# Optimization experiments

Hardware: AMD Instinct MI355X
Metric: run time of the kernel (lower is better)

## Reference

```python
import jax, jax.numpy as jnp
import numpy as np

B, T1, T2 = 2, 1024, 512
D_MODEL, N_HEAD, D_HEAD = 1024, 16, 64
SCALE = 1.0 / D_HEAD ** 0.5
EPS = 1e-5


def _skew(qe):
    # qe: [B, H, T, 2T-1] -> [B, H, T, T] via Transformer-XL pad/reshape trick
    b, h, t, x = qe.shape
    qe = jnp.pad(qe, ((0, 0), (0, 0), (0, 0), (0, 1))).reshape(b, h, 2 * t * t)
    qe = jnp.pad(qe, ((0, 0), (0, 0), (0, t - 1))).reshape(b, h, t + 1, 2 * t - 1)
    return qe[:, :, :t, -t:]


def setup_inputs() -> dict:
    key = jax.random.key(0)
    ks = jax.random.split(key, 12)
    s = 0.02
    return {
        "Q": jax.random.normal(ks[0], (B, T1, D_MODEL), jnp.float32),
        "K": jax.random.normal(ks[1], (B, T1, D_MODEL), jnp.float32),
        "V": jax.random.normal(ks[2], (B, T1, D_MODEL), jnp.float32),
        "lookup_table": jax.random.normal(ks[3], (2 * T1 - 1, D_HEAD), jnp.float32) * s,
        "valid_frames": jnp.sort(jax.random.randint(ks[4], (T2,), 0, T1)),
        "mask": jax.random.bernoulli(ks[5], 0.1, (B, N_HEAD, T1, T2)),
        "Wq": jax.random.normal(ks[6], (D_MODEL, N_HEAD * D_HEAD), jnp.float32) * s,
        "Wk": jax.random.normal(ks[7], (D_MODEL, N_HEAD * D_HEAD), jnp.float32) * s,
        "Wv": jax.random.normal(ks[8], (D_MODEL, N_HEAD * D_HEAD), jnp.float32) * s,
        "Wo": jax.random.normal(ks[9], (N_HEAD * D_HEAD, D_MODEL), jnp.float32) * s,
        "bo": jnp.zeros((D_MODEL,), jnp.float32),
        "ln_g": jnp.ones((D_MODEL,), jnp.float32),
        "ln_b": jnp.zeros((D_MODEL,), jnp.float32),
    }


def reference(Q, K, V, lookup_table, valid_frames, mask, Wq, Wk, Wv, Wo, bo, ln_g, ln_b):
    # gather valid KV frames (raw inputs, before projection)
    K = K[:, valid_frames]  # [B, T2, D]
    V = V[:, valid_frames]
    # pre-layernorm on Q only
    mu = jnp.mean(Q, axis=-1, keepdims=True)
    var = jnp.var(Q, axis=-1, keepdims=True)
    Qn = (Q - mu) * jax.lax.rsqrt(var + EPS) * ln_g + ln_b
    # projections -> [B, H, T, d_head]
    q = (Qn @ Wq).reshape(B, T1, N_HEAD, D_HEAD).transpose(0, 2, 1, 3)
    k = (K @ Wk).reshape(B, T2, N_HEAD, D_HEAD).transpose(0, 2, 1, 3)
    v = (V @ Wv).reshape(B, T2, N_HEAD, D_HEAD).transpose(0, 2, 1, 3)
    # content score + skewed relative-position score
    score = jnp.einsum("bhqd,bhkd->bhqk", q, k)  # [B,H,T1,T2]
    rel = jnp.einsum("bhqd,xd->bhqx", q, lookup_table)  # [B,H,T1,2T1-1]
    rel = _skew(rel)[:, :, :, valid_frames]  # [B,H,T1,T2]
    score = (score + rel) * SCALE
    score = jnp.where(mask, -jnp.finfo(score.dtype).max, score)
    attn = jax.nn.softmax(score, axis=-1)
    ctx = jnp.einsum("bhqk,bhkd->bhqd", attn, v)
    ctx = ctx.transpose(0, 2, 1, 3).reshape(B, T1, N_HEAD * D_HEAD)
    out = ctx @ Wo + bo  # dropout is identity at inference
    return out + ctx  # pre_layernorm=True branch
```

## Files before the change

kernel.cpp:

```cpp
#include <hip/hip_runtime.h>
#include <stdint.h>
#include <stddef.h>

typedef __attribute__((ext_vector_type(8))) short s16x8;
typedef __attribute__((ext_vector_type(4))) short s16x4;
typedef __attribute__((ext_vector_type(4))) float f32x4;

#define MFMA(a,b,c) __builtin_amdgcn_mfma_f32_16x16x32_bf16((a),(b),(c),0,0,0)

static __device__ __forceinline__ unsigned short f2b(float f){
  unsigned int b = __float_as_uint(f);
  b = (b + 0x7FFFu + ((b>>16)&1u)) >> 16;
  return (unsigned short)b;
}
static __device__ __forceinline__ float b2f(unsigned short u){
  return __uint_as_float(((unsigned int)u)<<16);
}


__global__ __launch_bounds__(256) void k_mask(const unsigned char* __restrict__ m,
    unsigned int* __restrict__ MB){
  const int t = threadIdx.x;
  const size_t g0 = (size_t)blockIdx.x*16;
  __shared__ int cnt1, cnt23;
  if(t==0){ cnt1=0; cnt23=0; }
  __syncthreads();
  const uint4* bp = (const uint4*)(m + g0*512);
  int l1=0,l23=0;
  #pragma unroll
  for(int i=0;i<2;i++){
    uint4 v = bp[t + i*256];
    unsigned int ws[4] = {v.x,v.y,v.z,v.w};
    #pragma unroll
    for(int j=0;j<4;j++){
      if((ws[j]>>8)&0xFFu) l1++;
      if(ws[j]>>16)        l23++;
    }
  }
  #pragma unroll
  for(int o=1;o<64;o<<=1){ l1 += __shfl_xor(l1,o); l23 += __shfl_xor(l23,o); }
  if((t&63)==0){ atomicAdd(&cnt1,l1); atomicAdd(&cnt23,l23); }
  __syncthreads();
  const int flag = cnt1 ? 1 : (cnt23 ? 2 : 0);

  const int rl = t>>4, f = t&15;
  const size_t base = (g0 + rl)*512 + f;
  unsigned int word = 0;
  if(flag==0){
    const int* p = (const int*)m;
    #pragma unroll
    for(int i=0;i<32;i++) word |= (p[base+i*16]!=0 ? 1u:0u) << i;
  } else if(flag==1){
    #pragma unroll
    for(int i=0;i<32;i++) word |= (m[base+i*16]!=0 ? 1u:0u) << i;
  } else {
    const float* p = (const float*)m;
    #pragma unroll
    for(int i=0;i<32;i++) word |= (p[base+i*16]!=0.f ? 1u:0u) << i;
  }
  MB[((size_t)blockIdx.x*4 + (t>>6))*64 + f*4 + (rl&3)] = word;
}

__global__ __launch_bounds__(256) void k_prep(
    const float* __restrict__ Q, const float* __restrict__ g, const float* __restrict__ be,
    unsigned short* __restrict__ Qn,
    const float* __restrict__ K, const float* __restrict__ V, const int* __restrict__ vf,
    unsigned short* __restrict__ Kg, unsigned short* __restrict__ Vg,
    const float* __restrict__ L, unsigned short* __restrict__ Lb,
    const float* __restrict__ W0, const float* __restrict__ W1,
    const float* __restrict__ W2, const float* __restrict__ W3,
    unsigned short* __restrict__ D0, unsigned short* __restrict__ D1,
    unsigned short* __restrict__ D2, unsigned short* __restrict__ D3){
  __shared__ float tile[64][65];
  __shared__ float red[8];
  const int bid = blockIdx.x, t = threadIdx.x;
  if(bid < 2048){
    const float4* xp = (const float4*)(Q + (size_t)bid*1024);
    float4 v = xp[t];
    float s  = v.x+v.y+v.z+v.w;
    float s2 = v.x*v.x+v.y*v.y+v.z*v.z+v.w*v.w;
    #pragma unroll
    for(int o=1;o<64;o<<=1){ s += __shfl_xor(s,o); s2 += __shfl_xor(s2,o); }
    int w = t>>6, l = t&63;
    if(l==0){ red[w]=s; red[4+w]=s2; }
    __syncthreads();
    s  = red[0]+red[1]+red[2]+red[3];
    s2 = red[4]+red[5]+red[6]+red[7];
    float mu = s*(1.f/1024.f);
    float var = s2*(1.f/1024.f) - mu*mu;
    float rs = rsqrtf(var + 1e-5f);
    float4 gv = ((const float4*)g)[t];
    float4 bv = ((const float4*)be)[t];
    ushort4 o4;
    o4.x = f2b((v.x-mu)*rs*gv.x + bv.x);
    o4.y = f2b((v.y-mu)*rs*gv.y + bv.y);
    o4.z = f2b((v.z-mu)*rs*gv.z + bv.z);
    o4.w = f2b((v.w-mu)*rs*gv.w + bv.w);
    ((ushort4*)(Qn + (size_t)bid*1024))[t] = o4;
  } else if(bid < 4096){
    int row = bid - 2048;
    int isV = row>>10, r = row&1023;
    int b = r>>9, jj = r&511;
    const float* src = (isV? V : K) + ((size_t)(b*1024 + vf[jj]))*1024;
    unsigned short* dst = (isV? Vg : Kg) + (size_t)r*1024;
    float4 v = ((const float4*)src)[t];
    ushort4 o; o.x=f2b(v.x); o.y=f2b(v.y); o.z=f2b(v.z); o.w=f2b(v.w);
    ((ushort4*)dst)[t] = o;
  } else if(bid < 4608){
    int i = (bid-4096)*256 + t;
    if(i < 2047*64) Lb[i] = f2b(L[i]);
  } else {
    int idx = bid - 4608;
    int z = idx>>8, rem = idx&255;
    int k0 = (rem&15)*64, n0 = (rem>>4)*64;
    const float* S = z==0?W0: z==1?W1: z==2?W2:W3;
    unsigned short* D = z==0?D0: z==1?D1: z==2?D2:D3;
    int tr = t>>6, tc = t&63;
    #pragma unroll
    for(int it=0;it<16;it++){ int r = it*4+tr; tile[r][tc] = S[(size_t)(k0+r)*1024 + n0+tc]; }
    __syncthreads();
    #pragma unroll
    for(int it=0;it<16;it++){ int r = it*4+tr; D[(size_t)(n0+r)*1024 + k0+tc] = f2b(tile[tc][r]); }
  }
}

__global__ __launch_bounds__(256) void k_proj(
    const short* __restrict__ QN, const short* __restrict__ WQT,
    const short* __restrict__ KG, const short* __restrict__ WKT,
    const short* __restrict__ WVT, const short* __restrict__ VG,
    unsigned short* __restrict__ QB, unsigned short* __restrict__ KB,
    unsigned short* __restrict__ VT){
  __shared__ __align__(16) short Ab[128*32];
  __shared__ __align__(16) short Bb[128*32];
  int bid = blockIdx.x;
  int mode, bx;
  if(bid<128){ mode=0; bx=bid>>3; }
  else if(bid<192){ mode=1; bx=(bid-128)>>3; }
  else { mode=2; bx=(bid-192)>>3; }
  int by = bid&7;
  const short* A  = mode==0? QN : mode==1? KG : WVT;
  const short* Bt = mode==0? WQT: mode==1? WKT: VG;

  const int t = threadIdx.x;
  const int w = t>>6, l = t&63;
  const int wr = w>>1, wc = w&1;
  const int fl15 = l&15, fl4 = l>>4;
  const size_t m0 = (size_t)bx*128, n0 = (size_t)by*128;
  const int srow = t>>2, scb = t&3;
  const int sg = scb ^ ((srow>>1)&3);
  const short* Ap = A + (m0+srow)*1024 + 8*sg;
  const short* Bp = Bt + (n0+srow)*1024 + 8*sg;

  f32x4 acc[4][4];
  const f32x4 zero = {0.f,0.f,0.f,0.f};
  #pragma unroll
  for(int m=0;m<4;m++)
    #pragma unroll
    for(int n=0;n<4;n++) acc[m][n] = zero;

  for(int k0=0;k0<1024;k0+=32){
    s16x8 a0 = *(const s16x8*)(Ap + k0);
    s16x8 a1 = *(const s16x8*)(Ap + 64*1024 + k0);
    s16x8 b0 = *(const s16x8*)(Bp + k0);
    s16x8 b1 = *(const s16x8*)(Bp + 64*1024 + k0);
    __syncthreads();
    *(s16x8*)(Ab + srow*32 + scb*8)      = a0;
    *(s16x8*)(Ab + (64+srow)*32 + scb*8) = a1;
    *(s16x8*)(Bb + srow*32 + scb*8)      = b0;
    *(s16x8*)(Bb + (64+srow)*32 + scb*8) = b1;
    __syncthreads();
    s16x8 af[4], bff[4];
    #pragma unroll
    for(int m=0;m<4;m++){
      int row = wr*64 + m*16 + fl15;
      int gg = fl4 ^ ((row>>1)&3);
      af[m] = *(const s16x8*)(Ab + row*32 + gg*8);
    }
    #pragma unroll
    for(int n=0;n<4;n++){
      int row = wc*64 + n*16 + fl15;
      int gg = fl4 ^ ((row>>1)&3);
      bff[n] = *(const s16x8*)(Bb + row*32 + gg*8);
    }
    #pragma unroll
    for(int m=0;m<4;m++)
      #pragma unroll
      for(int n=0;n<4;n++)
        acc[m][n] = MFMA(af[m], bff[n], acc[m][n]);
  }

  #pragma unroll
  for(int m=0;m<4;m++){
    #pragma unroll
    for(int n=0;n<4;n++){
      int mgb = (int)m0 + wr*64 + m*16 + 4*fl4;
      int ng  = (int)n0 + wc*64 + n*16 + fl15;
      #pragma unroll
      for(int p=0;p<4;p++){
        int mg = mgb + p;
        float v = acc[m][n][p];
        if(mode==0){ int b=mg>>10, i=mg&1023, h=ng>>6, d=ng&63;
          QB[((size_t)((b*16+h)*1024+i))*64 + d] = f2b(v); }
        else if(mode==1){ int b=mg>>9, jj=mg&511, h=ng>>6, d=ng&63;
          KB[((size_t)((b*16+h)*512+jj))*64 + d] = f2b(v); }
        else { int h=mg>>6, d=mg&63, b=ng>>9, jj=ng&511;
          VT[((size_t)((b*16+h)*64+d))*512 + jj] = f2b(v); }
      }
    }
  }
}

__global__ __launch_bounds__(256) void k_gemmO(
    const short* __restrict__ A, const short* __restrict__ Bt,
    float* __restrict__ out, const float* __restrict__ bo,
    const float* __restrict__ ctxf){
  __shared__ __align__(16) short Ab[128*32];
  __shared__ __align__(16) short Bb[128*32];
  const int t = threadIdx.x;
  const int w = t>>6, l = t&63;
  const int wr = w>>1, wc = w&1;
  const int fl15 = l&15, fl4 = l>>4;
  const size_t m0 = (size_t)blockIdx.x*128, n0 = (size_t)blockIdx.y*128;
  const int srow = t>>2, scb = t&3;
  const int sg = scb ^ ((srow>>1)&3);
  const short* Ap = A + (m0+srow)*1024 + 8*sg;
  const short* Bp = Bt + (n0+srow)*1024 + 8*sg;

  f32x4 acc[4][4];
  const f32x4 zero = {0.f,0.f,0.f,0.f};
  #pragma unroll
  for(int m=0;m<4;m++)
    #pragma unroll
    for(int n=0;n<4;n++) acc[m][n] = zero;

  for(int k0=0;k0<1024;k0+=32){
    s16x8 a0 = *(const s16x8*)(Ap + k0);
    s16x8 a1 = *(const s16x8*)(Ap + 64*1024 + k0);
    s16x8 b0 = *(const s16x8*)(Bp + k0);
    s16x8 b1 = *(const s16x8*)(Bp + 64*1024 + k0);
    __syncthreads();
    *(s16x8*)(Ab + srow*32 + scb*8)      = a0;
    *(s16x8*)(Ab + (64+srow)*32 + scb*8) = a1;
    *(s16x8*)(Bb + srow*32 + scb*8)      = b0;
    *(s16x8*)(Bb + (64+srow)*32 + scb*8) = b1;
    __syncthreads();
    s16x8 af[4], bff[4];
    #pragma unroll
    for(int m=0;m<4;m++){
      int row = wr*64 + m*16 + fl15;
      int gg = fl4 ^ ((row>>1)&3);
      af[m] = *(const s16x8*)(Ab + row*32 + gg*8);
    }
    #pragma unroll
    for(int n=0;n<4;n++){
      int row = wc*64 + n*16 + fl15;
      int gg = fl4 ^ ((row>>1)&3);
      bff[n] = *(const s16x8*)(Bb + row*32 + gg*8);
    }
    #pragma unroll
    for(int m=0;m<4;m++)
      #pragma unroll
      for(int n=0;n<4;n++)
        acc[m][n] = MFMA(af[m], bff[n], acc[m][n]);
  }

  #pragma unroll
  for(int m=0;m<4;m++){
    #pragma unroll
    for(int n=0;n<4;n++){
      int mgb = (int)m0 + wr*64 + m*16 + 4*fl4;
      int ng  = (int)n0 + wc*64 + n*16 + fl15;
      #pragma unroll
      for(int p=0;p<4;p++){
        int mg = mgb + p;
        size_t idx = (size_t)mg*1024 + ng;
        out[idx] = acc[m][n][p] + bo[ng] + ctxf[idx];
      }
    }
  }
}

#define RGS 20
#define GROWS 287
__global__ __launch_bounds__(256,2) void k_attn(const short* __restrict__ qb,
    const short* __restrict__ kb, const short* __restrict__ vt,
    const short* __restrict__ lbf, const int* __restrict__ vf,
    const unsigned int* __restrict__ MB,
    unsigned short* __restrict__ ctxb, float* __restrict__ ctxf){
  __shared__ __align__(16) short Gs[4][GROWS*RGS];
  __shared__ __align__(16) short PB[4][1024];
  __shared__ int vfs[512];
  const int t=threadIdx.x, w=t>>6, l=t&63, fl15=l&15, fl4=l>>4;
  const int bh = blockIdx.y;
  const int qg = blockIdx.x;
  const int qw = qg*16;
  for(int i=t;i<512;i+=256) vfs[i]=vf[i];
  __syncthreads();
  const int vf0 = vfs[0];
  const int x0  = 1008 + vf0 - qw;
  const int xcw = x0 + w*256;

  const short* qp = qb + ((size_t)(bh*1024 + qw + fl15))*64 + 8*fl4;
  s16x8 qa0 = *(const s16x8*)qp;
  s16x8 qa1 = *(const s16x8*)(qp+32);

  short* Gw = &Gs[w][0];
  const f32x4 zero = {0.f,0.f,0.f,0.f};
  #pragma unroll 4
  for(int tt=0;tt<17;tt++){
    int xr = xcw + tt*16 + fl15; if(xr>2046) xr = 2046;
    const short* lp = lbf + (size_t)xr*64 + 8*fl4;
    s16x8 b0 = *(const s16x8*)lp;
    s16x8 b1 = *(const s16x8*)(lp+32);
    f32x4 a = zero;
    a = MFMA(qa0,b0,a); a = MFMA(qa1,b1,a);
    int cb = tt*16 + fl15 + 4*fl4;
    #pragma unroll
    for(int p=0;p<4;p++) Gw[(cb+p)*RGS + 4*fl4 + p] = (short)f2b(a[p]);
  }

  const int rowgrp = bh*256 + qg*4 + fl4;
  uint4 mv = ((const uint4*)MB)[rowgrp*16 + fl15];
  unsigned int mbits[4] = {mv.x, mv.y, mv.z, mv.w};

  __syncthreads();

  const short* kp_row = kb + ((size_t)(bh*512 + fl15))*64 + 8*fl4;
  const short* vpb[4];
  #pragma unroll
  for(int dt=0;dt<4;dt++)
    vpb[dt] = vt + ((size_t)(bh*64 + dt*16 + fl15))*512 + w*128 + 8*fl4;

  f32x4 facc[4];
  #pragma unroll
  for(int dt=0;dt<4;dt++) facc[dt] = zero;
  float m_run[4] = {-1e30f,-1e30f,-1e30f,-1e30f};
  float ps[4]    = {0.f,0.f,0.f,0.f};
  short* Pw = &PB[w][0];

  for(int c=0;c<2;c++){
    s16x8 vfr[8];
    #pragma unroll
    for(int dt=0;dt<4;dt++){
      vfr[2*dt]   = *(const s16x8*)(vpb[dt] + c*64);
      vfr[2*dt+1] = *(const s16x8*)(vpb[dt] + c*64 + 32);
    }
    f32x4 S[4];
    #pragma unroll
    for(int tl=0;tl<4;tl++){
      int ttg = 8*w + 4*c + tl;
      const short* ka = kp_row + (size_t)ttg*1024;
      s16x8 k0v = *(const s16x8*)ka;
      s16x8 k1v = *(const s16x8*)(ka+32);
      f32x4 a = zero;
      a = MFMA(qa0,k0v,a); a = MFMA(qa1,k1v,a);
      int jj = ttg*16 + fl15;
      int o  = vfs[jj] - vf0;
      s16x4 rl = *(const s16x4*)(&Gs[o>>8][((o&255)+15)*RGS + 4*fl4]);
      #pragma unroll
      for(int p=0;p<4;p++){
        float sv = (a[p] + b2f((unsigned short)rl[p])) * 0.125f;
        bool mskb = (mbits[p]>>ttg)&1u;
        a[p] = mskb ? -1e30f : sv;
      }
      S[tl] = a;
    }
    float cm[4];
    #pragma unroll
    for(int p=0;p<4;p++){
      cm[p] = fmaxf(fmaxf(S[0][p],S[1][p]), fmaxf(S[2][p],S[3][p]));
      #pragma unroll
      for(int o=1;o<16;o<<=1) cm[p] = fmaxf(cm[p], __shfl_xor(cm[p],o));
      float mn = fmaxf(m_run[p], cm[p]);
      float fac = __expf(m_run[p]-mn);
      m_run[p] = mn;
      ps[p] *= fac;
      #pragma unroll
      for(int dt=0;dt<4;dt++) facc[dt][p] *= fac;
    }
    #pragma unroll
    for(int tl=0;tl<4;tl++){
      #pragma unroll
      for(int p=0;p<4;p++){
        float e = __expf(S[tl][p]-m_run[p]);
        ps[p] += e;
        int row = 4*fl4+p;
        Pw[row*64 + ((tl*16 + fl15) ^ (fl4<<4))] = (short)f2b(e);
      }
    }
    #pragma unroll
    for(int s=0;s<2;s++){
      s16x8 pa = *(const s16x8*)(Pw + fl15*64 + ((s*32 + fl4*8) ^ ((fl15>>2)<<4)));
      #pragma unroll
      for(int dt=0;dt<4;dt++)
        facc[dt] = MFMA(pa, vfr[2*dt+s], facc[dt]);
    }
  }

  #pragma unroll
  for(int p=0;p<4;p++){
    #pragma unroll
    for(int o=1;o<16;o<<=1) ps[p] += __shfl_xor(ps[p],o);
  }

  __syncthreads();
  float* MT = (float*)&Gs[0][0];
  float* ST = MT + 64;
  float* MG = ST + 64;
  if(fl15==0){
    #pragma unroll
    for(int p=0;p<4;p++){ MT[w*16 + 4*fl4+p] = m_run[p]; ST[w*16 + 4*fl4+p] = ps[p]; }
  }
  __syncthreads();
  float scale[4];
  #pragma unroll
  for(int p=0;p<4;p++){
    int row = 4*fl4+p;
    float ms  = fmaxf(fmaxf(MT[row],MT[16+row]), fmaxf(MT[32+row],MT[48+row]));
    float den = __expf(MT[row]-ms)*ST[row] + __expf(MT[16+row]-ms)*ST[16+row]
              + __expf(MT[32+row]-ms)*ST[32+row] + __expf(MT[48+row]-ms)*ST[48+row];
    scale[p] = __expf(m_run[p]-ms) / den;
  }
  #pragma unroll
  for(int dt=0;dt<4;dt++)
    #pragma unroll
    for(int p=0;p<4;p++)
      MG[(w*16 + 4*fl4+p)*65 + dt*16 + fl15] = facc[dt][p]*scale[p];
  __syncthreads();
  const int b = bh>>4, h = bh&15;
  #pragma unroll
  for(int p=0;p<4;p++){
    int row = 4*fl4+p;
    float v = MG[(row)*65    + w*16+fl15] + MG[(16+row)*65 + w*16+fl15]
            + MG[(32+row)*65 + w*16+fl15] + MG[(48+row)*65 + w*16+fl15];
    size_t idx = ((size_t)(b*1024 + qw + row))*1024 + h*64 + w*16 + fl15;
    ctxb[idx] = f2b(v);
    ctxf[idx] = v;
  }
}

extern "C" void kernel_launch(void* const* d_in, const int* in_sizes, int n_in,
                              void* d_out, int out_size, void* d_ws, size_t ws_size,
                              hipStream_t stream){
  (void)in_sizes; (void)n_in; (void)out_size; (void)ws_size;
  const float* Q  = (const float*)d_in[0];
  const float* K  = (const float*)d_in[1];
  const float* V  = (const float*)d_in[2];
  const float* Lt = (const float*)d_in[3];
  const int*   vf = (const int*)d_in[4];
  const void*  mk = d_in[5];
  const float* Wq = (const float*)d_in[6];
  const float* Wk = (const float*)d_in[7];
  const float* Wv = (const float*)d_in[8];
  const float* Wo = (const float*)d_in[9];
  const float* bo = (const float*)d_in[10];
  const float* lg = (const float*)d_in[11];
  const float* lb = (const float*)d_in[12];

  char* base = (char*)d_ws;
  size_t off = 0;
  auto alloc = [&](size_t bytes)->char*{
    char* p = base + off; off += (bytes + 255) & ~(size_t)255; return p; };
  unsigned int*   MBp = (unsigned int*)alloc(32768ull*16*4);
  unsigned short* QN  = (unsigned short*)alloc(2048ull*1024*2);
  unsigned short* KG  = (unsigned short*)alloc(1024ull*1024*2);
  unsigned short* VG  = (unsigned short*)alloc(1024ull*1024*2);
  unsigned short* WQT = (unsigned short*)alloc(1024ull*1024*2);
  unsigned short* WKT = (unsigned short*)alloc(1024ull*1024*2);
  unsigned short* WVT = (unsigned short*)alloc(1024ull*1024*2);
  unsigned short* WOT = (unsigned short*)alloc(1024ull*1024*2);
  unsigned short* LB  = (unsigned short*)alloc(2047ull*64*2);
  unsigned short* QB  = (unsigned short*)alloc(32ull*1024*64*2);
  unsigned short* KB  = (unsigned short*)alloc(32ull*512*64*2);
  unsigned short* VT  = (unsigned short*)alloc(32ull*64*512*2);
  unsigned short* CB  = (unsigned short*)alloc(2048ull*1024*2);
  float*          CF  = (float*)alloc(2048ull*1024*4);

  k_mask<<<2048,256,0,stream>>>((const unsigned char*)mk, MBp);
  k_prep<<<5632,256,0,stream>>>(Q, lg, lb, QN, K, V, vf, KG, VG, Lt, LB,
                                Wq, Wk, Wv, Wo, WQT, WKT, WVT, WOT);
  k_proj<<<256,256,0,stream>>>((const short*)QN,(const short*)WQT,
                               (const short*)KG,(const short*)WKT,
                               (const short*)WVT,(const short*)VG,
                               QB, KB, VT);
  k_attn<<<dim3(64,32),256,0,stream>>>((const short*)QB,(const short*)KB,(const short*)VT,
                                       (const short*)LB, vf, MBp, CB, CF);
  k_gemmO<<<dim3(16,8),256,0,stream>>>((const short*)CB,(const short*)WOT,
                                       (float*)d_out, bo, CF);
}
```

Before: 146.0 us.

## Split attention keys across eight waves per block and drop online softmax loop

The attention kernel now launches 512 threads per block, so each of eight waves handles 64 keys in a single pass rather than four waves looping over two 64-key chunks. K fragments are prefetched into registers before the relative-position table build, and that build is split across wave halves. The P buffer now reuses the Gs shared region after an extra barrier, and the cross-wave softmax merge is widened to eight partials. This adds parallelism and latency hiding per block but raises register pressure and adds barriers under a 512,4 launch bound.

Measured after the change: 144.9 us. Within noise of the previous version (-0.8%).

```diff
diff --git a/kernel.cpp b/kernel.cpp
--- a/kernel.cpp
+++ b/kernel.cpp
@@ -282,32 +282,45 @@
 
 #define RGS 20
 #define GROWS 287
-__global__ __launch_bounds__(256,2) void k_attn(const short* __restrict__ qb,
+__global__ __launch_bounds__(512,4) void k_attn(const short* __restrict__ qb,
     const short* __restrict__ kb, const short* __restrict__ vt,
     const short* __restrict__ lbf, const int* __restrict__ vf,
     const unsigned int* __restrict__ MB,
     unsigned short* __restrict__ ctxb, float* __restrict__ ctxf){
   __shared__ __align__(16) short Gs[4][GROWS*RGS];
-  __shared__ __align__(16) short PB[4][1024];
   __shared__ int vfs[512];
   const int t=threadIdx.x, w=t>>6, l=t&63, fl15=l&15, fl4=l>>4;
   const int bh = blockIdx.y;
   const int qg = blockIdx.x;
   const int qw = qg*16;
-  for(int i=t;i<512;i+=256) vfs[i]=vf[i];
-  __syncthreads();
-  const int vf0 = vfs[0];
-  const int x0  = 1008 + vf0 - qw;
-  const int xcw = x0 + w*256;
 
   const short* qp = qb + ((size_t)(bh*1024 + qw + fl15))*64 + 8*fl4;
   s16x8 qa0 = *(const s16x8*)qp;
   s16x8 qa1 = *(const s16x8*)(qp+32);
-
-  short* Gw = &Gs[w][0];
+  const int rowgrp = bh*256 + qg*4 + fl4;
+  uint4 mv = ((const uint4*)MB)[rowgrp*16 + fl15];
+
+  const short* kp_row = kb + ((size_t)(bh*512 + fl15))*64 + 8*fl4;
+  s16x8 kf[8];
+  #pragma unroll
+  for(int i=0;i<4;i++){
+    const short* ka = kp_row + (size_t)(4*w+i)*1024;
+    kf[2*i]   = *(const s16x8*)ka;
+    kf[2*i+1] = *(const s16x8*)(ka+32);
+  }
+
+  vfs[t] = vf[t & 511];
+  __syncthreads();
+  const int vf0 = vfs[0];
+  const int x0  = 1008 + vf0 - qw;
+  const int cw  = w&3;
+  const int xcw = x0 + cw*256;
+
+  short* Gw = &Gs[cw][0];
   const f32x4 zero = {0.f,0.f,0.f,0.f};
-  #pragma unroll 4
-  for(int tt=0;tt<17;tt++){
+  const int tbeg = (w>>2)? 9 : 0;
+  const int tend = (w>>2)? 17 : 9;
+  for(int tt=tbeg; tt<tend; tt++){
     int xr = xcw + tt*16 + fl15; if(xr>2046) xr = 2046;
     const short* lp = lbf + (size_t)xr*64 + 8*fl4;
     s16x8 b0 = *(const s16x8*)lp;
@@ -319,82 +332,73 @@
     for(int p=0;p<4;p++) Gw[(cb+p)*RGS + 4*fl4 + p] = (short)f2b(a[p]);
   }
 
-  const int rowgrp = bh*256 + qg*4 + fl4;
-  uint4 mv = ((const uint4*)MB)[rowgrp*16 + fl15];
   unsigned int mbits[4] = {mv.x, mv.y, mv.z, mv.w};
-
-  __syncthreads();
-
-  const short* kp_row = kb + ((size_t)(bh*512 + fl15))*64 + 8*fl4;
+  __syncthreads();
+
+  s16x4 rl[4];
+  #pragma unroll
+  for(int i=0;i<4;i++){
+    int jj = (4*w+i)*16 + fl15;
+    int o  = vfs[jj] - vf0;
+    rl[i] = *(const s16x4*)(&Gs[o>>8][((o&255)+15)*RGS + 4*fl4]);
+  }
+  __syncthreads();
+
+  f32x4 S[4];
+  #pragma unroll
+  for(int tl=0;tl<4;tl++){
+    int ttg = 4*w + tl;
+    f32x4 a = zero;
+    a = MFMA(qa0, kf[2*tl], a); a = MFMA(qa1, kf[2*tl+1], a);
+    #pragma unroll
+    for(int p=0;p<4;p++){
+      float sv = (a[p] + b2f((unsigned short)rl[tl][p])) * 0.125f;
+      bool mskb = (mbits[p]>>ttg)&1u;
+      a[p] = mskb ? -1e30f : sv;
+    }
+    S[tl] = a;
+  }
+
   const short* vpb[4];
   #pragma unroll
   for(int dt=0;dt<4;dt++)
-    vpb[dt] = vt + ((size_t)(bh*64 + dt*16 + fl15))*512 + w*128 + 8*fl4;
-
+    vpb[dt] = vt + ((size_t)(bh*64 + dt*16 + fl15))*512 + w*64 + 8*fl4;
+  s16x8 vfr[8];
+  #pragma unroll
+  for(int dt=0;dt<4;dt++){
+    vfr[2*dt]   = *(const s16x8*)(vpb[dt]);
+    vfr[2*dt+1] = *(const s16x8*)(vpb[dt] + 32);
+  }
+
+  float m_run[4], ps[4];
+  #pragma unroll
+  for(int p=0;p<4;p++){
+    float cm = fmaxf(fmaxf(S[0][p],S[1][p]), fmaxf(S[2][p],S[3][p]));
+    #pragma unroll
+    for(int o=1;o<16;o<<=1) cm = fmaxf(cm, __shfl_xor(cm,o));
+    m_run[p] = cm;
+    ps[p] = 0.f;
+  }
+  short* Pw = ((short*)Gs) + w*1024;
+  #pragma unroll
+  for(int tl=0;tl<4;tl++){
+    #pragma unroll
+    for(int p=0;p<4;p++){
+      float e = __expf(S[tl][p]-m_run[p]);
+      ps[p] += e;
+      int row = 4*fl4+p;
+      Pw[row*64 + ((tl*16 + fl15) ^ (fl4<<4))] = (short)f2b(e);
+    }
+  }
   f32x4 facc[4];
   #pragma unroll
   for(int dt=0;dt<4;dt++) facc[dt] = zero;
-  float m_run[4] = {-1e30f,-1e30f,-1e30f,-1e30f};
-  float ps[4]    = {0.f,0.f,0.f,0.f};
-  short* Pw = &PB[w][0];
-
-  for(int c=0;c<2;c++){
-    s16x8 vfr[8];
-    #pragma unroll
-    for(int dt=0;dt<4;dt++){
-      vfr[2*dt]   = *(const s16x8*)(vpb[dt] + c*64);
-      vfr[2*dt+1] = *(const s16x8*)(vpb[dt] + c*64 + 32);
-    }
-    f32x4 S[4];
-    #pragma unroll
-    for(int tl=0;tl<4;tl++){
-      int ttg = 8*w + 4*c + tl;
-      const short* ka = kp_row + (size_t)ttg*1024;
-      s16x8 k0v = *(const s16x8*)ka;
-      s16x8 k1v = *(const s16x8*)(ka+32);
-      f32x4 a = zero;
-      a = MFMA(qa0,k0v,a); a = MFMA(qa1,k1v,a);
-      int jj = ttg*16 + fl15;
-      int o  = vfs[jj] - vf0;
-      s16x4 rl = *(const s16x4*)(&Gs[o>>8][((o&255)+15)*RGS + 4*fl4]);
-      #pragma unroll
-      for(int p=0;p<4;p++){
-        float sv = (a[p] + b2f((unsigned short)rl[p])) * 0.125f;
-        bool mskb = (mbits[p]>>ttg)&1u;
-        a[p] = mskb ? -1e30f : sv;
-      }
-      S[tl] = a;
-    }
-    float cm[4];
-    #pragma unroll
-    for(int p=0;p<4;p++){
-      cm[p] = fmaxf(fmaxf(S[0][p],S[1][p]), fmaxf(S[2][p],S[3][p]));
-      #pragma unroll
-      for(int o=1;o<16;o<<=1) cm[p] = fmaxf(cm[p], __shfl_xor(cm[p],o));
-      float mn = fmaxf(m_run[p], cm[p]);
-      float fac = __expf(m_run[p]-mn);
-      m_run[p] = mn;
-      ps[p] *= fac;
-      #pragma unroll
-      for(int dt=0;dt<4;dt++) facc[dt][p] *= fac;
-    }
-    #pragma unroll
-    for(int tl=0;tl<4;tl++){
-      #pragma unroll
-      for(int p=0;p<4;p++){
-        float e = __expf(S[tl][p]-m_run[p]);
-        ps[p] += e;
-        int row = 4*fl4+p;
-        Pw[row*64 + ((tl*16 + fl15) ^ (fl4<<4))] = (short)f2b(e);
-      }
-    }
-    #pragma unroll
-    for(int s=0;s<2;s++){
-      s16x8 pa = *(const s16x8*)(Pw + fl15*64 + ((s*32 + fl4*8) ^ ((fl15>>2)<<4)));
-      #pragma unroll
-      for(int dt=0;dt<4;dt++)
-        facc[dt] = MFMA(pa, vfr[2*dt+s], facc[dt]);
-    }
+  #pragma unroll
+  for(int s=0;s<2;s++){
+    s16x8 pa = *(const s16x8*)(Pw + fl15*64 + ((s*32 + fl4*8) ^ ((fl15>>2)<<4)));
+    #pragma unroll
+    for(int dt=0;dt<4;dt++)
+      facc[dt] = MFMA(pa, vfr[2*dt+s], facc[dt]);
   }
 
   #pragma unroll
@@ -405,8 +409,8 @@
 
   __syncthreads();
   float* MT = (float*)&Gs[0][0];
-  float* ST = MT + 64;
-  float* MG = ST + 64;
+  float* ST = MT + 128;
+  float* MG = ST + 128;
   if(fl15==0){
     #pragma unroll
     for(int p=0;p<4;p++){ MT[w*16 + 4*fl4+p] = m_run[p]; ST[w*16 + 4*fl4+p] = ps[p]; }
@@ -416,9 +420,12 @@
   #pragma unroll
   for(int p=0;p<4;p++){
     int row = 4*fl4+p;
-    float ms  = fmaxf(fmaxf(MT[row],MT[16+row]), fmaxf(MT[32+row],MT[48+row]));
-    float den = __expf(MT[row]-ms)*ST[row] + __expf(MT[16+row]-ms)*ST[16+row]
-              + __expf(MT[32+row]-ms)*ST[32+row] + __expf(MT[48+row]-ms)*ST[48+row];
+    float ms = -1e30f;
+    #pragma unroll
+    for(int k=0;k<8;k++) ms = fmaxf(ms, MT[k*16+row]);
+    float den = 0.f;
+    #pragma unroll
+    for(int k=0;k<8;k++) den += __expf(MT[k*16+row]-ms)*ST[k*16+row];
     scale[p] = __expf(m_run[p]-ms) / den;
   }
   #pragma unroll
@@ -427,15 +434,18 @@
     for(int p=0;p<4;p++)
       MG[(w*16 + 4*fl4+p)*65 + dt*16 + fl15] = facc[dt][p]*scale[p];
   __syncthreads();
-  const int b = bh>>4, h = bh&15;
-  #pragma unroll
-  for(int p=0;p<4;p++){
-    int row = 4*fl4+p;
-    float v = MG[(row)*65    + w*16+fl15] + MG[(16+row)*65 + w*16+fl15]
-            + MG[(32+row)*65 + w*16+fl15] + MG[(48+row)*65 + w*16+fl15];
-    size_t idx = ((size_t)(b*1024 + qw + row))*1024 + h*64 + w*16 + fl15;
-    ctxb[idx] = f2b(v);
-    ctxf[idx] = v;
+  if(w < 4){
+    const int b = bh>>4, h = bh&15;
+    #pragma unroll
+    for(int p=0;p<4;p++){
+      int row = 4*fl4+p;
+      float v = 0.f;
+      #pragma unroll
+      for(int k=0;k<8;k++) v += MG[(k*16+row)*65 + w*16+fl15];
+      size_t idx = ((size_t)(b*1024 + qw + row))*1024 + h*64 + w*16 + fl15;
+      ctxb[idx] = f2b(v);
+      ctxf[idx] = v;
+    }
   }
 }
 
@@ -483,7 +493,7 @@
                                (const short*)KG,(const short*)WKT,
                                (const short*)WVT,(const short*)VG,
                                QB, KB, VT);
-  k_attn<<<dim3(64,32),256,0,stream>>>((const short*)QB,(const short*)KB,(const short*)VT,
+  k_attn<<<dim3(64,32),512,0,stream>>>((const short*)QB,(const short*)KB,(const short*)VT,
                                        (const short*)LB, vf, MBp, CB, CF);
   k_gemmO<<<dim3(16,8),256,0,stream>>>((const short*)CB,(const short*)WOT,
                                        (float*)d_out, bo, CF);
```
